# Optimization experiments

Measured on AMD Instinct MI355X. Metric: run time of the kernel, lower is better.

Reference implementation:

```python
import jax, jax.numpy as jnp
import numpy as np

N_HEADS = 32
N_KV_HEADS = 8
HEAD_DIM = 128
N_REP = N_HEADS // N_KV_HEADS


def apply_rope(x, cos, sin):
    # x: [B, S, H, D]; cos/sin: [S_max, D//2]
    S = x.shape[1]
    c = cos[:S][None, :, None, :]
    s = sin[:S][None, :, None, :]
    x_even = x[..., ::2]
    x_odd = x[..., 1::2]
    out = jnp.stack([x_even * c - x_odd * s, x_even * s + x_odd * c], axis=-1)
    return out.reshape(x.shape)


def setup_inputs() -> dict:
    key = jax.random.key(0)
    ks = jax.random.split(key, 8)
    B, S, D = 2, 2048, 4096
    x = jax.random.normal(ks[0], (B, S, D), dtype=jnp.float32)
    # RoPE tables
    pos = jnp.arange(S, dtype=jnp.float32)[:, None]
    inv_freq = 1.0 / (10000.0 ** (jnp.arange(0, HEAD_DIM, 2, dtype=jnp.float32) / HEAD_DIM))
    ang = pos * inv_freq[None, :]  # [S, HEAD_DIM//2]
    cos = jnp.cos(ang)
    sin = jnp.sin(ang)
    # causal additive mask [1,1,S,S]
    tril = jnp.tril(jnp.ones((S, S), dtype=bool))
    mask = jnp.where(tril, 0.0, -1e9).astype(jnp.float32)[None, None]
    sc = 0.02
    Wq = jax.random.normal(ks[1], (D, N_HEADS * HEAD_DIM), dtype=jnp.float32) * sc
    Wk = jax.random.normal(ks[2], (D, N_KV_HEADS * HEAD_DIM), dtype=jnp.float32) * sc
    Wv = jax.random.normal(ks[3], (D, N_KV_HEADS * HEAD_DIM), dtype=jnp.float32) * sc
    Wo = jax.random.normal(ks[4], (N_HEADS * HEAD_DIM, D), dtype=jnp.float32) * sc
    return {"x": x, "cos": cos, "sin": sin, "mask": mask,
            "Wq": Wq, "Wk": Wk, "Wv": Wv, "Wo": Wo}


def reference(x, cos, sin, mask, Wq, Wk, Wv, Wo):
    B, S, D = x.shape
    q = (x @ Wq).reshape(B, S, N_HEADS, HEAD_DIM)
    k = (x @ Wk).reshape(B, S, N_KV_HEADS, HEAD_DIM)
    v = (x @ Wv).reshape(B, S, N_KV_HEADS, HEAD_DIM)
    q = apply_rope(q, cos, sin)
    k = apply_rope(k, cos, sin)
    # repeat_interleave KV heads to match query heads
    k = jnp.repeat(k, N_REP, axis=2)
    v = jnp.repeat(v, N_REP, axis=2)
    q = q.transpose(0, 2, 1, 3)  # [B, H, S, D]
    k = k.transpose(0, 2, 1, 3)
    v = v.transpose(0, 2, 1, 3)
    scale = HEAD_DIM ** -0.5
    scores = jnp.einsum('bhqd,bhkd->bhqk', q, k) * scale + mask
    attn = jax.nn.softmax(scores, axis=-1)
    out = jnp.einsum('bhqk,bhkd->bhqd', attn, v)
    out = out.transpose(0, 2, 1, 3).reshape(B, S, N_HEADS * HEAD_DIM)
    return out @ Wo
```

## Files before the change

### kernel.cpp

```cpp
#include <hip/hip_runtime.h>

typedef __attribute__((ext_vector_type(8))) short short8;
typedef __attribute__((ext_vector_type(4))) float f32x4;
typedef __attribute__((ext_vector_type(4))) unsigned short u16x4;
typedef __attribute__((ext_vector_type(8))) unsigned short u16x8;

typedef __attribute__((address_space(3))) void lds_void;
typedef __attribute__((address_space(1))) void g_void;

#define GL16(g, l) __builtin_amdgcn_global_load_lds((g_void*)(g), (lds_void*)(l), 16, 0, 0)
#define EXP2F(x) __builtin_exp2f(x)
#define BARRIER() do { asm volatile("" ::: "memory"); __builtin_amdgcn_s_barrier(); asm volatile("" ::: "memory"); } while (0)

__device__ inline float b2f(unsigned short u) {
  union { unsigned u; float f; } v; v.u = ((unsigned)u) << 16; return v.f;
}
__device__ inline unsigned short f2b(float f) {
  union { float f; unsigned u; } v; v.f = f;
  unsigned r = v.u + 0x7FFFu + ((v.u >> 16) & 1u);
  return (unsigned short)(r >> 16);
}
__device__ inline unsigned short f2b_rne(float f) {
  unsigned u;
  asm("v_cvt_pk_bf16_f32 %0, %1, %2" : "=v"(u) : "v"(f), "v"(f));
  return (unsigned short)u;
}
__device__ inline unsigned short cvtb(float v) { return f2b(v); }
__device__ inline unsigned short cvtb(unsigned short v) { return v; }

__global__ __launch_bounds__(256) void conv_f32_bf16(const float* __restrict__ in,
                                                     unsigned short* __restrict__ out, long n) {
  long i = ((long)blockIdx.x * 256 + threadIdx.x) * 4;
  if (i >= n) return;
  f32x4 v = *(const f32x4*)(in + i);
  u16x4 o;
  o[0] = f2b(v[0]); o[1] = f2b(v[1]); o[2] = f2b(v[2]); o[3] = f2b(v[3]);
  *(u16x4*)(out + i) = o;
}

template <typename TIN>
__global__ __launch_bounds__(256) void transpose_bf16(const TIN* __restrict__ in,
                                                      unsigned short* __restrict__ out,
                                                      int R, int C, int ldin) {
  __shared__ unsigned short tile[32][33];
  int c0 = blockIdx.x * 32, r0 = blockIdx.y * 32;
  int tx = threadIdx.x & 31, ty = threadIdx.x >> 5;
#pragma unroll
  for (int i = ty; i < 32; i += 8)
    tile[i][tx] = cvtb(in[(long)(r0 + i) * ldin + c0 + tx]);
  __syncthreads();
#pragma unroll
  for (int i = ty; i < 32; i += 8)
    out[(long)(c0 + i) * R + r0 + tx] = tile[tx][i];
}

template <int MODE>
__global__ __launch_bounds__(256, 2) void gemm128(const unsigned short* __restrict__ A,
                                                  const unsigned short* __restrict__ Bt,
                                                  void* __restrict__ C,
                                                  const float* __restrict__ cosp,
                                                  const float* __restrict__ sinp,
                                                  int M, int N, int K) {
  __shared__ unsigned short As[2][128 * 64];
  __shared__ unsigned short Bs[2][128 * 64];
  const int tid = threadIdx.x;
  const int wid = tid >> 6, lane = tid & 63;
  const int lrow = lane & 15, kq = lane >> 4;
  const int wr = wid >> 1, wc = wid & 1;
  const int nbn = N >> 7;
  const int nwg = (M >> 7) * nbn;
  const int bid = blockIdx.x;
  const int swz = (bid & 7) * (nwg >> 3) + (bid >> 3);
  const int bm = swz / nbn, bn = swz % nbn;

  const long K2 = (long)K * 2;
  const long csw = (long)(((tid & 7) ^ ((tid >> 3) & 7)) << 4);
  const char* gA = (const char*)A + ((long)bm * 128 + (tid >> 3)) * K2 + csw;
  const char* gB = (const char*)Bt + ((long)bn * 128 + (tid >> 3)) * K2 + csw;

#define STAGEAB(buf, koff) do { \
    char* _da = (char*)As + (buf) * 16384 + tid * 16; \
    char* _db = (char*)Bs + (buf) * 16384 + tid * 16; \
    GL16(gA + (koff),               _da); \
    GL16(gA + (koff) + 32 * K2,     _da + 4096); \
    GL16(gA + (koff) + 64 * K2,     _da + 8192); \
    GL16(gA + (koff) + 96 * K2,     _da + 12288); \
    GL16(gB + (koff),               _db); \
    GL16(gB + (koff) + 32 * K2,     _db + 4096); \
    GL16(gB + (koff) + 64 * K2,     _db + 8192); \
    GL16(gB + (koff) + 96 * K2,     _db + 12288); } while (0)

  f32x4 acc[4][4];
#pragma unroll
  for (int m = 0; m < 4; m++)
#pragma unroll
    for (int n = 0; n < 4; n++) acc[m][n] = (f32x4){0.f, 0.f, 0.f, 0.f};

  const int arow = (wr * 64 + lrow) * 64;
  const int brow = (wc * 64 + lrow) * 64;
  const int ax = lrow & 7;

  STAGEAB(0, 0);

  const int NT = K >> 6;
  for (int t = 0; t < NT; ++t) {
    const int c = t & 1;
    BARRIER();
    if (t + 1 < NT) {
      STAGEAB(c ^ 1, (long)(t + 1) << 7);
      asm volatile("s_waitcnt vmcnt(8)" ::: "memory");
    } else {
      asm volatile("s_waitcnt vmcnt(0)" ::: "memory");
    }
    const unsigned short* Ab = As[0] + c * 8192;
    const unsigned short* Bb = Bs[0] + c * 8192;
    short8 af[4][2], bfv[4][2];
#pragma unroll
    for (int m = 0; m < 4; m++)
#pragma unroll
      for (int kk = 0; kk < 2; kk++)
        af[m][kk] = *(const short8*)&Ab[arow + m * 1024 + (((kk * 4 + kq) ^ ax) << 3)];
#pragma unroll
    for (int n = 0; n < 4; n++)
#pragma unroll
      for (int kk = 0; kk < 2; kk++)
        bfv[n][kk] = *(const short8*)&Bb[brow + n * 1024 + (((kk * 4 + kq) ^ ax) << 3)];
    __builtin_amdgcn_s_setprio(1);
#pragma unroll
    for (int m = 0; m < 4; m++)
#pragma unroll
      for (int n = 0; n < 4; n++)
#pragma unroll
        for (int kk = 0; kk < 2; kk++)
          acc[m][n] = __builtin_amdgcn_mfma_f32_16x16x32_bf16(af[m][kk], bfv[n][kk], acc[m][n], 0, 0, 0);
    __builtin_amdgcn_s_setprio(0);
  }
#undef STAGEAB

  const long crow0 = (long)bm * 128 + wr * 64 + kq * 4;
  const int ccol0 = bn * 128 + wc * 64 + lrow;
  const float qscale = 0.08838834764831845f * 1.44269504088896341f;
#pragma unroll
  for (int m = 0; m < 4; m++)
#pragma unroll
    for (int n = 0; n < 4; n++)
#pragma unroll
      for (int r = 0; r < 4; r++) {
        long row = crow0 + m * 16 + r;
        int col = ccol0 + n * 16;
        float v = acc[m][n][r];
        if (MODE == 0) {
          ((float*)C)[row * N + col] = v;
        } else {
          float other = __shfl_xor(v, 1, 64);
          float out = v;
          if (col < 5120) {
            int s = (int)(row & 2047);
            int ib = (col & 127) >> 1;
            float cc = cosp[s * 64 + ib], ss = sinp[s * 64 + ib];
            out = (col & 1) ? (other * ss + v * cc) : (v * cc - other * ss);
            if (col < 4096) out *= qscale;
          }
          ((unsigned short*)C)[row * N + col] = f2b(out);
        }
      }
}

__global__ __launch_bounds__(256) void attn_kernel(const unsigned short* __restrict__ QKV,
                                                   const unsigned short* __restrict__ Vt,
                                                   unsigned short* __restrict__ O,
                                                   int S, int BS) {
  __shared__ unsigned short Ks[64 * 128];
  __shared__ unsigned short Vs[128 * 64];
  __shared__ unsigned short Ps[4][16 * 68];
  const int tid = threadIdx.x, wave = tid >> 6, lane = tid & 63;
  const int lrow = lane & 15, kgrp = lane >> 4;
  const int nqt = S >> 6, nqt2 = nqt >> 1;
  int bid = blockIdx.x;
  const int qp = bid % nqt2; bid /= nqt2;
  const int h = bid & 31;
  const int b = bid >> 5;
  const int kh = h >> 2;
  const long rowbase = (long)b * S;

  const char* kg = (const char*)(QKV + rowbase * 6144 + 4096 + kh * 128)
                   + (tid >> 4) * 12288 + (((tid & 15) ^ ((tid >> 4) & 7)) * 16);
  const char* vg = (const char*)(Vt + (long)(kh * 128 + (tid >> 3)) * BS + rowbase)
                   + (((tid & 7) ^ ((tid >> 3) & 7)) * 16);
  char* lK = (char*)Ks + wave * 1024;
  char* lV = (char*)Vs + wave * 1024;

  for (int pass = 0; pass < 2; pass++) {
    const int qt = pass ? (nqt - 1 - qp) : qp;
    const int qbase = qt * 64;
    const int q0 = qbase + wave * 16;

    short8 qf[4];
    {
      const unsigned short* qpt = QKV + (rowbase + q0 + lrow) * 6144 + h * 128 + kgrp * 8;
#pragma unroll
      for (int dc = 0; dc < 4; dc++) qf[dc] = *(const short8*)(qpt + dc * 32);
    }
    f32x4 oacc[8];
#pragma unroll
    for (int dt = 0; dt < 8; dt++) oacc[dt] = (f32x4){0.f, 0.f, 0.f, 0.f};
    float mrun[4] = {-1e30f, -1e30f, -1e30f, -1e30f};
    float lrun[4] = {0.f, 0.f, 0.f, 0.f};

    const int kv_end = qbase + 64;
    for (int kv0 = 0; kv0 < kv_end; kv0 += 64) {
      __syncthreads();
#pragma unroll
      for (int p = 0; p < 4; p++)
        GL16(kg + (long)(kv0 + p * 16) * 12288, lK + p * 4096);
#pragma unroll
      for (int p = 0; p < 4; p++)
        GL16(vg + (long)kv0 * 2 + (long)p * 32 * BS * 2, lV + p * 4096);
      __syncthreads();

      f32x4 sc[4];
#pragma unroll
      for (int n = 0; n < 4; n++) {
        f32x4 s = (f32x4){0.f, 0.f, 0.f, 0.f};
#pragma unroll
        for (int dc = 0; dc < 4; dc++) {
          short8 kf = *(const short8*)(Ks + (n * 16 + lrow) * 128 + (((dc * 4 + kgrp) ^ (lrow & 7)) << 3));
          s = __builtin_amdgcn_mfma_f32_16x16x32_bf16(qf[dc], kf, s, 0, 0, 0);
        }
        sc[n] = s;
      }

      if (kv0 + 63 > q0) {
#pragma unroll
        for (int r = 0; r < 4; r++) {
          const int qg = q0 + kgrp * 4 + r;
#pragma unroll
          for (int n = 0; n < 4; n++) {
            int kgi = kv0 + n * 16 + lrow;
            if (kgi > qg) sc[n][r] = -1e30f;
          }
        }
      }

      float mx[4];
#pragma unroll
      for (int r = 0; r < 4; r++) {
        float m0 = fmaxf(fmaxf(sc[0][r], sc[1][r]), fmaxf(sc[2][r], sc[3][r]));
#pragma unroll
        for (int d = 1; d < 16; d <<= 1) m0 = fmaxf(m0, __shfl_xor(m0, d, 64));
        mx[r] = m0;
      }
      bool grow = false;
#pragma unroll
      for (int r = 0; r < 4; r++) grow = grow || (mx[r] > mrun[r] + 8.f);

      if (__all(!grow)) {
#pragma unroll
        for (int r = 0; r < 4; r++) {
          float psum = 0.f;
#pragma unroll
          for (int n = 0; n < 4; n++) {
            float pv = EXP2F(sc[n][r] - mrun[r]);
            psum += pv;
            Ps[wave][(kgrp * 4 + r) * 68 + n * 16 + lrow] = f2b_rne(pv);
          }
          lrun[r] += psum;
        }
      } else {
#pragma unroll
        for (int r = 0; r < 4; r++) {
          float mnew = fmaxf(mrun[r], mx[r]);
          float corr = EXP2F(mrun[r] - mnew);
          mrun[r] = mnew;
          float psum = 0.f;
#pragma unroll
          for (int n = 0; n < 4; n++) {
            float pv = EXP2F(sc[n][r] - mnew);
            psum += pv;
            Ps[wave][(kgrp * 4 + r) * 68 + n * 16 + lrow] = f2b_rne(pv);
          }
          lrun[r] = lrun[r] * corr + psum;
#pragma unroll
          for (int dt = 0; dt < 8; dt++) oacc[dt][r] *= corr;
        }
      }
      asm volatile("s_waitcnt lgkmcnt(0)" ::: "memory");
#pragma unroll
      for (int kc = 0; kc < 2; kc++) {
        short8 pa = *(const short8*)(&Ps[wave][lrow * 68 + kc * 32 + kgrp * 8]);
#pragma unroll
        for (int dt = 0; dt < 8; dt++) {
          short8 vb = *(const short8*)(Vs + (dt * 16 + lrow) * 64 + (((kc * 4 + kgrp) ^ (lrow & 7)) << 3));
          oacc[dt] = __builtin_amdgcn_mfma_f32_16x16x32_bf16(pa, vb, oacc[dt], 0, 0, 0);
        }
      }
    }

    float inv[4];
#pragma unroll
    for (int r = 0; r < 4; r++) {
      float l = lrun[r];
#pragma unroll
      for (int d = 1; d < 16; d <<= 1) l += __shfl_xor(l, d, 64);
      inv[r] = 1.f / l;
    }
    unsigned short* op = O + (rowbase + q0 + kgrp * 4) * 4096 + h * 128 + lrow;
#pragma unroll
    for (int dt = 0; dt < 8; dt++)
#pragma unroll
      for (int r = 0; r < 4; r++)
        op[(long)r * 4096 + dt * 16] = f2b_rne(oacc[dt][r] * inv[r]);
  }
}

extern "C" void kernel_launch(void* const* d_in, const int* in_sizes, int n_in,
                              void* d_out, int out_size, void* d_ws, size_t ws_size,
                              hipStream_t stream) {
  const float* x = (const float*)d_in[0];
  const float* cosp = (const float*)d_in[1];
  const float* sinp = (const float*)d_in[2];
  const float* Wq = (const float*)d_in[4];
  const float* Wk = (const float*)d_in[5];
  const float* Wv = (const float*)d_in[6];
  const float* Wo = (const float*)d_in[7];
  const int S = 2048;
  const long M = 4096;

  if (ws_size < 176160768ULL) return;

  char* ws = (char*)d_ws;
  unsigned short* xb   = (unsigned short*)(ws);
  unsigned short* Wqt  = (unsigned short*)(ws + 33554432);
  unsigned short* Wkt  = (unsigned short*)(ws + 67108864);
  unsigned short* Wvt  = (unsigned short*)(ws + 75497472);
  unsigned short* Wot  = (unsigned short*)(ws + 83886080);
  unsigned short* QKVb = (unsigned short*)(ws + 117440512);
  unsigned short* Vtg  = (unsigned short*)(ws + 167772160);
  unsigned short* AO   = xb;

  conv_f32_bf16<<<16384, 256, 0, stream>>>(x, xb, M * 4096);
  transpose_bf16<float><<<dim3(128, 128), 256, 0, stream>>>(Wq, Wqt, 4096, 4096, 4096);
  transpose_bf16<float><<<dim3(32, 128), 256, 0, stream>>>(Wk, Wkt, 4096, 1024, 1024);
  transpose_bf16<float><<<dim3(32, 128), 256, 0, stream>>>(Wv, Wvt, 4096, 1024, 1024);
  transpose_bf16<float><<<dim3(128, 128), 256, 0, stream>>>(Wo, Wot, 4096, 4096, 4096);

  gemm128<2><<<1536, 256, 0, stream>>>(xb, Wqt, QKVb, cosp, sinp, 4096, 6144, 4096);
  transpose_bf16<unsigned short><<<dim3(32, 128), 256, 0, stream>>>(QKVb + 5120, Vtg, 4096, 1024, 6144);

  attn_kernel<<<1024, 256, 0, stream>>>(QKVb, Vtg, AO, S, 4096);

  gemm128<0><<<1024, 256, 0, stream>>>(AO, Wot, d_out, nullptr, nullptr, 4096, 4096, 4096);
}
```

Before: 686.4 us.

## Replace 128x128 GEMM with 256x256-tile 8-wave kernel and 4-stage LDS ring

The projection GEMMs move from 128x128 tiles with 4 waves and a 2-stage double buffer to 256x256 tiles with 8 waves. Each wave computes a 128x64 sub-tile. K steps drop to 32 and run through a 4-deep LDS ring, with A and B loads issued separately and interleaved between the two MFMA halves. The aim is more data reuse per byte loaded and better hiding of global-load latency. The cost is more accumulator registers, more barriers per step, and far fewer workgroups (384 and 256), which may underfill the GPU's compute units.

After: 668.4 us. 2.6% less time.

```diff
diff --git a/kernel.cpp b/kernel.cpp
--- a/kernel.cpp
+++ b/kernel.cpp
@@ -55,100 +55,99 @@
 }
 
 template <int MODE>
-__global__ __launch_bounds__(256, 2) void gemm128(const unsigned short* __restrict__ A,
+__global__ __launch_bounds__(512, 2) void gemm_r4(const unsigned short* __restrict__ A,
                                                   const unsigned short* __restrict__ Bt,
                                                   void* __restrict__ C,
                                                   const float* __restrict__ cosp,
                                                   const float* __restrict__ sinp,
                                                   int M, int N, int K) {
-  __shared__ unsigned short As[2][128 * 64];
-  __shared__ unsigned short Bs[2][128 * 64];
+  __shared__ unsigned short L[4 * 16384];
   const int tid = threadIdx.x;
   const int wid = tid >> 6, lane = tid & 63;
   const int lrow = lane & 15, kq = lane >> 4;
-  const int wr = wid >> 1, wc = wid & 1;
-  const int nbn = N >> 7;
-  const int nwg = (M >> 7) * nbn;
+  const int wr = wid >> 2, wc = wid & 3;
+  const int nbn = N >> 8;
+  const int nwg = (M >> 8) * nbn;
   const int bid = blockIdx.x;
   const int swz = (bid & 7) * (nwg >> 3) + (bid >> 3);
   const int bm = swz / nbn, bn = swz % nbn;
 
   const long K2 = (long)K * 2;
-  const long csw = (long)(((tid & 7) ^ ((tid >> 3) & 7)) << 4);
-  const char* gA = (const char*)A + ((long)bm * 128 + (tid >> 3)) * K2 + csw;
-  const char* gB = (const char*)Bt + ((long)bn * 128 + (tid >> 3)) * K2 + csw;
-
-#define STAGEAB(buf, koff) do { \
-    char* _da = (char*)As + (buf) * 16384 + tid * 16; \
-    char* _db = (char*)Bs + (buf) * 16384 + tid * 16; \
-    GL16(gA + (koff),               _da); \
-    GL16(gA + (koff) + 32 * K2,     _da + 4096); \
-    GL16(gA + (koff) + 64 * K2,     _da + 8192); \
-    GL16(gA + (koff) + 96 * K2,     _da + 12288); \
-    GL16(gB + (koff),               _db); \
-    GL16(gB + (koff) + 32 * K2,     _db + 4096); \
-    GL16(gB + (koff) + 64 * K2,     _db + 8192); \
-    GL16(gB + (koff) + 96 * K2,     _db + 12288); } while (0)
-
-  f32x4 acc[4][4];
-#pragma unroll
-  for (int m = 0; m < 4; m++)
-#pragma unroll
-    for (int n = 0; n < 4; n++) acc[m][n] = (f32x4){0.f, 0.f, 0.f, 0.f};
-
-  const int arow = (wr * 64 + lrow) * 64;
-  const int brow = (wc * 64 + lrow) * 64;
-  const int ax = lrow & 7;
-
-  STAGEAB(0, 0);
-
-  const int NT = K >> 6;
+  const int csw = (tid & 3) ^ ((tid >> 3) & 3);
+  const char* gA = (const char*)A + ((long)bm * 256 + (tid >> 2)) * K2 + csw * 16;
+  const char* gB = (const char*)Bt + ((long)bn * 256 + (tid >> 2)) * K2 + csw * 16;
+
+#define STAGE_A(t) do { char* _d = (char*)L + ((t) & 3) * 32768 + tid * 16; \
+    const char* _s = gA + (long)(t) * 64; GL16(_s, _d); GL16(_s + 128 * K2, _d + 8192); } while (0)
+#define STAGE_B(t) do { char* _d = (char*)L + ((t) & 3) * 32768 + 16384 + tid * 16; \
+    const char* _s = gB + (long)(t) * 64; GL16(_s, _d); GL16(_s + 128 * K2, _d + 8192); } while (0)
+
+  f32x4 acc[8][4];
+#pragma unroll
+  for (int mf = 0; mf < 8; mf++)
+#pragma unroll
+    for (int nf = 0; nf < 4; nf++) acc[mf][nf] = (f32x4){0.f, 0.f, 0.f, 0.f};
+
+  const int rowA0 = wr * 128 + lrow, rowB0 = wc * 64 + lrow;
+  const int offA = rowA0 * 64 + ((kq ^ ((rowA0 >> 1) & 3)) << 4);
+  const int offB = 16384 + rowB0 * 64 + ((kq ^ ((rowB0 >> 1) & 3)) << 4);
+
+  STAGE_A(0); STAGE_B(0); STAGE_A(1); STAGE_B(1); STAGE_A(2); STAGE_B(2);
+  asm volatile("s_waitcnt vmcnt(8)" ::: "memory");
+  BARRIER();
+
+  const int NT = K >> 5;
+#pragma unroll 4
   for (int t = 0; t < NT; ++t) {
-    const int c = t & 1;
+    const char* Sb = (const char*)L + (t & 3) * 32768;
+    short8 bf[4], af[4];
+#pragma unroll
+    for (int nf = 0; nf < 4; nf++) bf[nf] = *(const short8*)(Sb + offB + nf * 1024);
+#pragma unroll
+    for (int j = 0; j < 4; j++) af[j] = *(const short8*)(Sb + offA + j * 1024);
+    if (t + 3 < NT) STAGE_A(t + 3);
     BARRIER();
-    if (t + 1 < NT) {
-      STAGEAB(c ^ 1, (long)(t + 1) << 7);
-      asm volatile("s_waitcnt vmcnt(8)" ::: "memory");
-    } else {
-      asm volatile("s_waitcnt vmcnt(0)" ::: "memory");
-    }
-    const unsigned short* Ab = As[0] + c * 8192;
-    const unsigned short* Bb = Bs[0] + c * 8192;
-    short8 af[4][2], bfv[4][2];
-#pragma unroll
-    for (int m = 0; m < 4; m++)
-#pragma unroll
-      for (int kk = 0; kk < 2; kk++)
-        af[m][kk] = *(const short8*)&Ab[arow + m * 1024 + (((kk * 4 + kq) ^ ax) << 3)];
-#pragma unroll
-    for (int n = 0; n < 4; n++)
-#pragma unroll
-      for (int kk = 0; kk < 2; kk++)
-        bfv[n][kk] = *(const short8*)&Bb[brow + n * 1024 + (((kk * 4 + kq) ^ ax) << 3)];
+    asm volatile("s_waitcnt lgkmcnt(0)" ::: "memory");
     __builtin_amdgcn_s_setprio(1);
 #pragma unroll
-    for (int m = 0; m < 4; m++)
-#pragma unroll
-      for (int n = 0; n < 4; n++)
-#pragma unroll
-        for (int kk = 0; kk < 2; kk++)
-          acc[m][n] = __builtin_amdgcn_mfma_f32_16x16x32_bf16(af[m][kk], bfv[n][kk], acc[m][n], 0, 0, 0);
+    for (int j = 0; j < 4; j++)
+#pragma unroll
+      for (int nf = 0; nf < 4; nf++)
+        acc[j][nf] = __builtin_amdgcn_mfma_f32_16x16x32_bf16(af[j], bf[nf], acc[j][nf], 0, 0, 0);
     __builtin_amdgcn_s_setprio(0);
+    BARRIER();
+#pragma unroll
+    for (int j = 0; j < 4; j++) af[j] = *(const short8*)(Sb + offA + (4 + j) * 1024);
+    if (t + 3 < NT) STAGE_B(t + 3);
+    BARRIER();
+    asm volatile("s_waitcnt lgkmcnt(0)" ::: "memory");
+    __builtin_amdgcn_s_setprio(1);
+#pragma unroll
+    for (int j = 0; j < 4; j++)
+#pragma unroll
+      for (int nf = 0; nf < 4; nf++)
+        acc[4 + j][nf] = __builtin_amdgcn_mfma_f32_16x16x32_bf16(af[j], bf[nf], acc[4 + j][nf], 0, 0, 0);
+    __builtin_amdgcn_s_setprio(0);
+    if (t + 4 < NT)      asm volatile("s_waitcnt vmcnt(8)" ::: "memory");
+    else if (t + 3 < NT) asm volatile("s_waitcnt vmcnt(4)" ::: "memory");
+    else                 asm volatile("s_waitcnt vmcnt(0)" ::: "memory");
+    BARRIER();
   }
-#undef STAGEAB
-
-  const long crow0 = (long)bm * 128 + wr * 64 + kq * 4;
-  const int ccol0 = bn * 128 + wc * 64 + lrow;
+#undef STAGE_A
+#undef STAGE_B
+
+  const long crow0 = (long)bm * 256 + wr * 128 + kq * 4;
+  const int ccol0 = bn * 256 + wc * 64 + lrow;
   const float qscale = 0.08838834764831845f * 1.44269504088896341f;
 #pragma unroll
-  for (int m = 0; m < 4; m++)
-#pragma unroll
-    for (int n = 0; n < 4; n++)
+  for (int mf = 0; mf < 8; mf++)
+#pragma unroll
+    for (int nf = 0; nf < 4; nf++)
 #pragma unroll
       for (int r = 0; r < 4; r++) {
-        long row = crow0 + m * 16 + r;
-        int col = ccol0 + n * 16;
-        float v = acc[m][n][r];
+        long row = crow0 + mf * 16 + r;
+        int col = ccol0 + nf * 16;
+        float v = acc[mf][nf][r];
         if (MODE == 0) {
           ((float*)C)[row * N + col] = v;
         } else {
@@ -344,10 +343,10 @@
   transpose_bf16<float><<<dim3(32, 128), 256, 0, stream>>>(Wv, Wvt, 4096, 1024, 1024);
   transpose_bf16<float><<<dim3(128, 128), 256, 0, stream>>>(Wo, Wot, 4096, 4096, 4096);
 
-  gemm128<2><<<1536, 256, 0, stream>>>(xb, Wqt, QKVb, cosp, sinp, 4096, 6144, 4096);
+  gemm_r4<2><<<384, 512, 0, stream>>>(xb, Wqt, QKVb, cosp, sinp, 4096, 6144, 4096);
   transpose_bf16<unsigned short><<<dim3(32, 128), 256, 0, stream>>>(QKVb + 5120, Vtg, 4096, 1024, 6144);
 
   attn_kernel<<<1024, 256, 0, stream>>>(QKVb, Vtg, AO, S, 4096);
 
-  gemm128<0><<<1024, 256, 0, stream>>>(AO, Wot, d_out, nullptr, nullptr, 4096, 4096, 4096);
-}
+  gemm_r4<0><<<256, 512, 0, stream>>>(AO, Wot, d_out, nullptr, nullptr, 4096, 4096, 4096);
+}
```

## Rewrite GEMM with 32x32x16 MFMA, single-buffered LDS, and three blocks per CU

Applied to the files above, without the earlier changes.

Replaces the double-buffered 16x16x32 MFMA GEMM with a single-buffered kernel that uses 32x32x16 bf16 MFMA, fewer LDS fragment reads per wave, and launch bounds allowing three workgroups per CU. It drops the L2-friendly block swizzle, the s_setprio hints and the overlap of global loads with compute, relying on occupancy to hide latency instead. It also switches the bf16 output conversion to the hardware round-to-nearest-even instruction. Removing the prefetch pipeline and the swizzle risks exposing memory latency and worse cache reuse.

Result: faster. 659.4 us (-3.9%).

```diff
diff --git a/kernel.cpp b/kernel.cpp
--- a/kernel.cpp
+++ b/kernel.cpp
@@ -2,6 +2,7 @@
 
 typedef __attribute__((ext_vector_type(8))) short short8;
 typedef __attribute__((ext_vector_type(4))) float f32x4;
+typedef __attribute__((ext_vector_type(16))) float f32x16;
 typedef __attribute__((ext_vector_type(4))) unsigned short u16x4;
 typedef __attribute__((ext_vector_type(8))) unsigned short u16x8;
 
@@ -10,7 +11,6 @@
 
 #define GL16(g, l) __builtin_amdgcn_global_load_lds((g_void*)(g), (lds_void*)(l), 16, 0, 0)
 #define EXP2F(x) __builtin_exp2f(x)
-#define BARRIER() do { asm volatile("" ::: "memory"); __builtin_amdgcn_s_barrier(); asm volatile("" ::: "memory"); } while (0)
 
 __device__ inline float b2f(unsigned short u) {
   union { unsigned u; float f; } v; v.u = ((unsigned)u) << 16; return v.f;
@@ -55,100 +55,80 @@
 }
 
 template <int MODE>
-__global__ __launch_bounds__(256, 2) void gemm128(const unsigned short* __restrict__ A,
-                                                  const unsigned short* __restrict__ Bt,
-                                                  void* __restrict__ C,
-                                                  const float* __restrict__ cosp,
-                                                  const float* __restrict__ sinp,
-                                                  int M, int N, int K) {
-  __shared__ unsigned short As[2][128 * 64];
-  __shared__ unsigned short Bs[2][128 * 64];
+__global__ __launch_bounds__(256, 3) void gemm_m97(const unsigned short* __restrict__ A,
+                                                   const unsigned short* __restrict__ Bt,
+                                                   void* __restrict__ C,
+                                                   const float* __restrict__ cosp,
+                                                   const float* __restrict__ sinp,
+                                                   int M, int N, int K) {
+  __shared__ unsigned short As[128 * 64];
+  __shared__ unsigned short Bs[128 * 64];
   const int tid = threadIdx.x;
-  const int wid = tid >> 6, lane = tid & 63;
-  const int lrow = lane & 15, kq = lane >> 4;
+  const int lane = tid & 63;
+  const int wid = tid >> 6;
   const int wr = wid >> 1, wc = wid & 1;
+  const int l31 = lane & 31, lh = lane >> 5;
+  const int xr = l31 & 7;
   const int nbn = N >> 7;
-  const int nwg = (M >> 7) * nbn;
-  const int bid = blockIdx.x;
-  const int swz = (bid & 7) * (nwg >> 3) + (bid >> 3);
-  const int bm = swz / nbn, bn = swz % nbn;
+  const int bm = blockIdx.x / nbn, bn = blockIdx.x % nbn;
 
   const long K2 = (long)K * 2;
-  const long csw = (long)(((tid & 7) ^ ((tid >> 3) & 7)) << 4);
+  const int csw = ((tid & 7) ^ ((tid >> 3) & 7)) << 4;
   const char* gA = (const char*)A + ((long)bm * 128 + (tid >> 3)) * K2 + csw;
   const char* gB = (const char*)Bt + ((long)bn * 128 + (tid >> 3)) * K2 + csw;
-
-#define STAGEAB(buf, koff) do { \
-    char* _da = (char*)As + (buf) * 16384 + tid * 16; \
-    char* _db = (char*)Bs + (buf) * 16384 + tid * 16; \
-    GL16(gA + (koff),               _da); \
-    GL16(gA + (koff) + 32 * K2,     _da + 4096); \
-    GL16(gA + (koff) + 64 * K2,     _da + 8192); \
-    GL16(gA + (koff) + 96 * K2,     _da + 12288); \
-    GL16(gB + (koff),               _db); \
-    GL16(gB + (koff) + 32 * K2,     _db + 4096); \
-    GL16(gB + (koff) + 64 * K2,     _db + 8192); \
-    GL16(gB + (koff) + 96 * K2,     _db + 12288); } while (0)
-
-  f32x4 acc[4][4];
-#pragma unroll
-  for (int m = 0; m < 4; m++)
-#pragma unroll
-    for (int n = 0; n < 4; n++) acc[m][n] = (f32x4){0.f, 0.f, 0.f, 0.f};
-
-  const int arow = (wr * 64 + lrow) * 64;
-  const int brow = (wc * 64 + lrow) * 64;
-  const int ax = lrow & 7;
-
-  STAGEAB(0, 0);
+  char* dA = (char*)As + tid * 16;
+  char* dB = (char*)Bs + tid * 16;
+
+  f32x16 acc[2][2];
+#pragma unroll
+  for (int m = 0; m < 2; m++)
+#pragma unroll
+    for (int n = 0; n < 2; n++)
+#pragma unroll
+      for (int i = 0; i < 16; i++) acc[m][n][i] = 0.f;
+
+  const int offA0 = (wr * 64 + l31) * 128;
+  const int offB0 = (wc * 64 + l31) * 128;
 
   const int NT = K >> 6;
   for (int t = 0; t < NT; ++t) {
-    const int c = t & 1;
-    BARRIER();
-    if (t + 1 < NT) {
-      STAGEAB(c ^ 1, (long)(t + 1) << 7);
-      asm volatile("s_waitcnt vmcnt(8)" ::: "memory");
-    } else {
-      asm volatile("s_waitcnt vmcnt(0)" ::: "memory");
+    __syncthreads();
+    const long ko = (long)t * 128;
+    GL16(gA + ko, dA);
+    GL16(gA + ko + 32 * K2, dA + 4096);
+    GL16(gA + ko + 64 * K2, dA + 8192);
+    GL16(gA + ko + 96 * K2, dA + 12288);
+    GL16(gB + ko, dB);
+    GL16(gB + ko + 32 * K2, dB + 4096);
+    GL16(gB + ko + 64 * K2, dB + 8192);
+    GL16(gB + ko + 96 * K2, dB + 12288);
+    __syncthreads();
+#pragma unroll
+    for (int kk = 0; kk < 4; kk++) {
+      const int co = (((kk * 2 + lh) ^ xr) << 4);
+      short8 a0 = *(const short8*)((const char*)As + offA0 + co);
+      short8 a1 = *(const short8*)((const char*)As + offA0 + 4096 + co);
+      short8 b0 = *(const short8*)((const char*)Bs + offB0 + co);
+      short8 b1 = *(const short8*)((const char*)Bs + offB0 + 4096 + co);
+      acc[0][0] = __builtin_amdgcn_mfma_f32_32x32x16_bf16(a0, b0, acc[0][0], 0, 0, 0);
+      acc[0][1] = __builtin_amdgcn_mfma_f32_32x32x16_bf16(a0, b1, acc[0][1], 0, 0, 0);
+      acc[1][0] = __builtin_amdgcn_mfma_f32_32x32x16_bf16(a1, b0, acc[1][0], 0, 0, 0);
+      acc[1][1] = __builtin_amdgcn_mfma_f32_32x32x16_bf16(a1, b1, acc[1][1], 0, 0, 0);
     }
-    const unsigned short* Ab = As[0] + c * 8192;
-    const unsigned short* Bb = Bs[0] + c * 8192;
-    short8 af[4][2], bfv[4][2];
-#pragma unroll
-    for (int m = 0; m < 4; m++)
-#pragma unroll
-      for (int kk = 0; kk < 2; kk++)
-        af[m][kk] = *(const short8*)&Ab[arow + m * 1024 + (((kk * 4 + kq) ^ ax) << 3)];
-#pragma unroll
-    for (int n = 0; n < 4; n++)
-#pragma unroll
-      for (int kk = 0; kk < 2; kk++)
-        bfv[n][kk] = *(const short8*)&Bb[brow + n * 1024 + (((kk * 4 + kq) ^ ax) << 3)];
-    __builtin_amdgcn_s_setprio(1);
-#pragma unroll
-    for (int m = 0; m < 4; m++)
-#pragma unroll
-      for (int n = 0; n < 4; n++)
-#pragma unroll
-        for (int kk = 0; kk < 2; kk++)
-          acc[m][n] = __builtin_amdgcn_mfma_f32_16x16x32_bf16(af[m][kk], bfv[n][kk], acc[m][n], 0, 0, 0);
-    __builtin_amdgcn_s_setprio(0);
   }
-#undef STAGEAB
-
-  const long crow0 = (long)bm * 128 + wr * 64 + kq * 4;
-  const int ccol0 = bn * 128 + wc * 64 + lrow;
+
+  const long crow0 = (long)bm * 128 + wr * 64 + 4 * lh;
+  const int ccol0 = bn * 128 + wc * 64 + l31;
   const float qscale = 0.08838834764831845f * 1.44269504088896341f;
 #pragma unroll
-  for (int m = 0; m < 4; m++)
-#pragma unroll
-    for (int n = 0; n < 4; n++)
-#pragma unroll
-      for (int r = 0; r < 4; r++) {
-        long row = crow0 + m * 16 + r;
-        int col = ccol0 + n * 16;
-        float v = acc[m][n][r];
+  for (int m = 0; m < 2; m++)
+#pragma unroll
+    for (int n = 0; n < 2; n++)
+#pragma unroll
+      for (int reg = 0; reg < 16; reg++) {
+        long row = crow0 + m * 32 + (reg & 3) + 8 * (reg >> 2);
+        int col = ccol0 + n * 32;
+        float v = acc[m][n][reg];
         if (MODE == 0) {
           ((float*)C)[row * N + col] = v;
         } else {
@@ -161,7 +141,7 @@
             out = (col & 1) ? (other * ss + v * cc) : (v * cc - other * ss);
             if (col < 4096) out *= qscale;
           }
-          ((unsigned short*)C)[row * N + col] = f2b(out);
+          ((unsigned short*)C)[row * N + col] = f2b_rne(out);
         }
       }
 }
@@ -344,10 +324,10 @@
   transpose_bf16<float><<<dim3(32, 128), 256, 0, stream>>>(Wv, Wvt, 4096, 1024, 1024);
   transpose_bf16<float><<<dim3(128, 128), 256, 0, stream>>>(Wo, Wot, 4096, 4096, 4096);
 
-  gemm128<2><<<1536, 256, 0, stream>>>(xb, Wqt, QKVb, cosp, sinp, 4096, 6144, 4096);
+  gemm_m97<2><<<1536, 256, 0, stream>>>(xb, Wqt, QKVb, cosp, sinp, 4096, 6144, 4096);
   transpose_bf16<unsigned short><<<dim3(32, 128), 256, 0, stream>>>(QKVb + 5120, Vtg, 4096, 1024, 6144);
 
   attn_kernel<<<1024, 256, 0, stream>>>(QKVb, Vtg, AO, S, 4096);
 
-  gemm128<0><<<1024, 256, 0, stream>>>(AO, Wot, d_out, nullptr, nullptr, 4096, 4096, 4096);
-}
+  gemm_m97<0><<<1024, 256, 0, stream>>>(AO, Wot, d_out, nullptr, nullptr, 4096, 4096, 4096);
+}
```
